# Kernel optimization log

Hardware: AMD Instinct MI355X
Metric: run time of the kernel (lower is better)

The kernel has to match this reference:

```python
import jax, jax.numpy as jnp
import numpy as np

POOL_RAD = 1.0   # init kwarg pool_rad
N = 16384        # total points
B = 8            # graphs in batch
F = 128          # feature dim
BIG = 1e30

def _voxel_keys(pos, batch, rad):
    # torch_geometric.voxel_grid with start=min-rad/2, end=max+rad/2, batch as extra dim
    start = pos.min(0) - rad * 0.5
    end = pos.max(0) + rad * 0.5
    nv = jnp.floor((end - start) / rad).astype(jnp.int32) + 1  # voxels per spatial dim
    c = jnp.floor((pos - start) / rad).astype(jnp.int32)       # [N,3] voxel coords
    lin = c[:, 0] + c[:, 1] * nv[0] + c[:, 2] * nv[0] * nv[1]
    return lin + batch.astype(jnp.int32) * (nv[0] * nv[1] * nv[2])

def _consecutive(keys, n):
    # consecutive_cluster: relabel to sorted-consecutive ids; perm = last index per cluster
    _, inv = jnp.unique(keys, return_inverse=True, size=n,
                        fill_value=jnp.iinfo(jnp.int32).max)
    inv = inv.reshape(-1)
    perm = jax.ops.segment_max(jnp.arange(n, dtype=jnp.int32), inv, num_segments=n)
    counts = jax.ops.segment_sum(jnp.ones((n,), jnp.int32), inv, num_segments=n)
    return inv, jnp.clip(perm, 0, n - 1), counts

def _nearest(pos, batch, cpos, cbatch, cvalid):
    # nearest centroid within the same graph; invalid/padded centroids masked out
    d = (pos * pos).sum(1)[:, None] - 2.0 * (pos @ cpos.T) + (cpos * cpos).sum(1)[None, :]
    ok = (batch[:, None] == cbatch[None, :]) & cvalid[None, :]
    return jnp.argmin(jnp.where(ok, d, BIG), axis=1)

def _pool(pos, x, batch):
    n = pos.shape[0]
    # stage 1: voxel-grid clustering, centroid positions
    inv1, perm1, cnt1 = _consecutive(_voxel_keys(pos, batch, POOL_RAD), n)
    c1 = jnp.maximum(cnt1, 1).astype(pos.dtype)[:, None]
    cpos = jax.ops.segment_sum(pos, inv1, num_segments=n) / c1
    cbatch = batch[perm1]
    # stage 2: reassign each point to its nearest voxel centroid, relabel
    cl2 = _nearest(jax.lax.stop_gradient(pos), batch,
                   jax.lax.stop_gradient(cpos), cbatch, cnt1 > 0)
    inv2, perm2, cnt2 = _consecutive(cl2, n)
    valid2 = cnt2 > 0
    c2 = jnp.maximum(cnt2, 1).astype(pos.dtype)[:, None]
    pos_out = jax.ops.segment_sum(pos, inv2, num_segments=n) / c2   # mean pos
    x_out = jax.ops.segment_max(x, inv2, num_segments=n)            # aggr='max'
    x_out = jnp.where(valid2[:, None], x_out, 0.0)
    pos_out = jnp.where(valid2[:, None], pos_out, 0.0)
    batch_out = jnp.where(valid2, batch[perm2], -1)
    return x_out, pos_out, batch_out

def setup_inputs():
    key = jax.random.key(0)
    k1, k2 = jax.random.split(key)
    pos = jax.random.uniform(k1, (N, 3), jnp.float32) * 10.0
    x = jax.random.normal(k2, (N, F), jnp.float32)
    batch = jnp.repeat(jnp.arange(B, dtype=jnp.int32), N // B)
    return {"pos": pos, "x": x, "batch": batch}

def reference(pos, x, batch):
    return _pool(pos, x, batch)
```

## Files before the change

### kernel.cpp

```cpp
#include <hip/hip_runtime.h>

#define TPB 256
#define K1SZ 32768

static __device__ __forceinline__ unsigned int fmap(float f) {
  unsigned int b = __float_as_uint(f);
  return (b & 0x80000000u) ? ~b : (b | 0x80000000u);
}
static __device__ __forceinline__ float funmap(unsigned int u) {
  unsigned int b = (u & 0x80000000u) ? (u & 0x7fffffffu) : ~u;
  return __uint_as_float(b);
}

static __device__ __forceinline__ int wave_incl_scan(int v, int lane) {
  #pragma unroll
  for (int off = 1; off < 64; off <<= 1) {
    int u = __shfl_up(v, off);
    if (lane >= off) v += u;
  }
  return v;
}

__global__ void k_init(double* __restrict__ sum1, double* __restrict__ sum2,
                       int* __restrict__ cnt1, int* __restrict__ cnt2,
                       int* __restrict__ perm2, int* __restrict__ flags1,
                       int* __restrict__ flags2, uint4* __restrict__ xacc4,
                       const float* __restrict__ pos, const int* __restrict__ batch,
                       float* __restrict__ scal, int n, int nF4) {
  int t = blockIdx.x * blockDim.x + threadIdx.x;
  if (t < nF4) xacc4[t] = uint4{0u, 0u, 0u, 0u};
  if (t < 3 * n) { sum1[t] = 0.0; sum2[t] = 0.0; }
  if (t < n) { cnt1[t] = 0; cnt2[t] = 0; perm2[t] = -1; flags2[t] = 0; }
  if (t < K1SZ) flags1[t] = 0;

  if (blockIdx.x == 0) {
    const int tid = threadIdx.x;
    const int lane = tid & 63, wid = tid >> 6;
    float mn[3] = {3.4e38f, 3.4e38f, 3.4e38f};
    float mx[3] = {-3.4e38f, -3.4e38f, -3.4e38f};
    int mb = 0;
    const float4* p4 = (const float4*)pos;
    const int4* b4 = (const int4*)batch;
    int np4 = n >> 2;
    for (int j = tid; j < np4; j += TPB) {
      float4 a = p4[3 * j], b = p4[3 * j + 1], c = p4[3 * j + 2];
      mn[0] = fminf(mn[0], fminf(fminf(a.x, a.w), fminf(b.z, c.y)));
      mx[0] = fmaxf(mx[0], fmaxf(fmaxf(a.x, a.w), fmaxf(b.z, c.y)));
      mn[1] = fminf(mn[1], fminf(fminf(a.y, b.x), fminf(b.w, c.z)));
      mx[1] = fmaxf(mx[1], fmaxf(fmaxf(a.y, b.x), fmaxf(b.w, c.z)));
      mn[2] = fminf(mn[2], fminf(fminf(a.z, b.y), fminf(c.x, c.w)));
      mx[2] = fmaxf(mx[2], fmaxf(fmaxf(a.z, b.y), fmaxf(c.x, c.w)));
      int4 bb = b4[j];
      mb = max(mb, max(max(bb.x, bb.y), max(bb.z, bb.w)));
    }
    if (tid == 0) {
      for (int i = np4 * 4; i < n; ++i) {
        for (int d = 0; d < 3; ++d) {
          float v = pos[i * 3 + d];
          mn[d] = fminf(mn[d], v);
          mx[d] = fmaxf(mx[d], v);
        }
        mb = max(mb, batch[i]);
      }
    }
    #pragma unroll
    for (int off = 32; off > 0; off >>= 1) {
      #pragma unroll
      for (int d = 0; d < 3; ++d) {
        mn[d] = fminf(mn[d], __shfl_xor(mn[d], off));
        mx[d] = fmaxf(mx[d], __shfl_xor(mx[d], off));
      }
      mb = max(mb, __shfl_xor(mb, off));
    }
    __shared__ float smn[4][3], smx[4][3];
    __shared__ int smb[4];
    if (lane == 0) {
      for (int d = 0; d < 3; ++d) { smn[wid][d] = mn[d]; smx[wid][d] = mx[d]; }
      smb[wid] = mb;
    }
    __syncthreads();
    if (tid == 0) {
      float rmn[3], rmx[3];
      int rmb = smb[0];
      for (int d = 0; d < 3; ++d) { rmn[d] = smn[0][d]; rmx[d] = smx[0][d]; }
      for (int w = 1; w < 4; ++w) {
        for (int d = 0; d < 3; ++d) {
          rmn[d] = fminf(rmn[d], smn[w][d]);
          rmx[d] = fmaxf(rmx[d], smx[w][d]);
        }
        rmb = max(rmb, smb[w]);
      }
      int nv[3];
      for (int d = 0; d < 3; ++d) {
        float start = rmn[d] - 0.5f;
        float end   = rmx[d] + 0.5f;
        nv[d] = (int)floorf(end - start) + 1;
        scal[d] = start;
      }
      int* isc = (int*)(scal + 3);
      isc[0] = nv[0];
      isc[1] = nv[0] * nv[1];
      isc[2] = nv[0] * nv[1] * nv[2];
      isc[3] = nv[1];
      isc[4] = nv[2];
      isc[5] = rmb + 1;
    }
  }
}

__global__ void k_keys(const float* __restrict__ pos, const int* __restrict__ batch, int n,
                       const float* __restrict__ scal, int* __restrict__ key1,
                       int* __restrict__ flags1) {
  int i = blockIdx.x * blockDim.x + threadIdx.x;
  if (i >= n) return;
  const int* isc = (const int*)(scal + 3);
  int c0 = (int)floorf(pos[i * 3 + 0] - scal[0]);
  int c1 = (int)floorf(pos[i * 3 + 1] - scal[1]);
  int c2 = (int)floorf(pos[i * 3 + 2] - scal[2]);
  int key = c0 + c1 * isc[0] + c2 * isc[1] + batch[i] * isc[2];
  key = min(max(key, 0), K1SZ - 1);
  key1[i] = key;
  flags1[key] = 1;
}

static __device__ __forceinline__ int scan_body(const int* __restrict__ flags,
                                                int* __restrict__ rank,
                                                int ntiles, int n4full, int* wsum) {
  const int t = threadIdx.x;
  const int lane = t & 63;
  const int wid = t >> 6;
  const int4* f4 = (const int4*)flags;
  int4* r4 = (int4*)rank;
  int base = 0;
  for (int tile = 0; tile < ntiles; ++tile) {
    int i = tile * 1024 + t;
    int4 v = (i < n4full) ? f4[i] : int4{0, 0, 0, 0};
    int q0 = v.x, q1 = q0 + v.y, q2 = q1 + v.z, q3 = q2 + v.w;
    int ws = wave_incl_scan(q3, lane);
    if (lane == 63) wsum[wid] = ws;
    __syncthreads();
    int woff = 0, ttot = 0;
    #pragma unroll
    for (int w = 0; w < 16; ++w) {
      int s = wsum[w];
      if (w < wid) woff += s;
      ttot += s;
    }
    int e = base + woff + (ws - q3);
    if (i < n4full) r4[i] = int4{e, e + q0, e + q1, e + q2};
    base += ttot;
    __syncthreads();
  }
  return base;
}

__global__ __launch_bounds__(1024) void k_scan1(const int* __restrict__ flags,
                                                int* __restrict__ rank,
                                                const float* __restrict__ scal) {
  __shared__ int wsum[16];
  const int* isc = (const int*)(scal + 3);
  long long L = (long long)isc[5] * isc[2];
  int L_eff = (int)(L > K1SZ ? K1SZ : L);
  int ntiles = (L_eff + 4095) >> 12;
  int base = scan_body(flags, rank, ntiles, K1SZ >> 2, wsum);
  if (threadIdx.x == 0) rank[K1SZ] = base;
}

__global__ __launch_bounds__(1024) void k_scan2(const int* __restrict__ flags,
                                                int* __restrict__ rank,
                                                const int* __restrict__ total1, int n) {
  __shared__ int wsum[16];
  int L_eff = min(n, *total1);
  int ntiles = (L_eff + 4095) >> 12;
  scan_body(flags, rank, ntiles, n >> 2, wsum);
}

__global__ void k_assign1(const float* __restrict__ pos, int n,
                          const int* __restrict__ key1, const int* __restrict__ rank1,
                          int* __restrict__ cnt1, double* __restrict__ sum1) {
  int i = blockIdx.x * blockDim.x + threadIdx.x;
  if (i >= n) return;
  int c = rank1[key1[i]];
  atomicAdd(&cnt1[c], 1);
  atomicAdd(&sum1[c * 3 + 0], (double)pos[i * 3 + 0]);
  atomicAdd(&sum1[c * 3 + 1], (double)pos[i * 3 + 1]);
  atomicAdd(&sum1[c * 3 + 2], (double)pos[i * 3 + 2]);
}

__global__ void k_nearest(const float* __restrict__ pos, const int* __restrict__ batch, int n,
                          const double* __restrict__ sum1, const int* __restrict__ cnt1,
                          const int* __restrict__ flags1, const int* __restrict__ rank1,
                          const float* __restrict__ scal,
                          int* __restrict__ cl2, int* __restrict__ flags2) {
  int i = blockIdx.x * blockDim.x + threadIdx.x;
  if (i >= n) return;
  const int* isc = (const int*)(scal + 3);
  const float s0 = scal[0], s1 = scal[1], s2 = scal[2];
  const int nv0 = isc[0], nv01 = isc[1], nvtot = isc[2];
  const int nv1 = isc[3], nv2 = isc[4];
  float pxf = pos[i * 3 + 0], pyf = pos[i * 3 + 1], pzf = pos[i * 3 + 2];
  double px = pxf, py = pyf, pz = pzf;
  int c0 = (int)floorf(pxf - s0);
  int c1 = (int)floorf(pyf - s1);
  int c2 = (int)floorf(pzf - s2);
  int base = batch[i] * nvtot;
  int k0 = min(max(c0 + c1 * nv0 + c2 * nv01 + base, 0), K1SZ - 1);
  int bid = rank1[k0];
  {
    double inv = 1.0 / (double)cnt1[bid];
    double dx = px - sum1[bid * 3 + 0] * inv;
    double dy = py - sum1[bid * 3 + 1] * inv;
    double dz = pz - sum1[bid * 3 + 2] * inv;
    double d2 = dx * dx + dy * dy + dz * dz;
    double best2 = d2;
    for (int oz = -2; oz <= 2; ++oz) {
      int z = c2 + oz;
      if (z < 0 || z >= nv2) continue;
      double lz = (double)s2 + z;
      double gz = fmax(0.0, fmax(lz - pz, pz - (lz + 1.0)));
      double gz2 = gz * gz;
      if (gz2 > best2 + 1e-4) continue;
      for (int oy = -2; oy <= 2; ++oy) {
        int y = c1 + oy;
        if (y < 0 || y >= nv1) continue;
        double ly = (double)s1 + y;
        double gy = fmax(0.0, fmax(ly - py, py - (ly + 1.0)));
        double gzy2 = gz2 + gy * gy;
        if (gzy2 > best2 + 1e-4) continue;
        for (int ox = -2; ox <= 2; ++ox) {
          int xq = c0 + ox;
          if (xq < 0 || xq >= nv0) continue;
          if ((ox | oy | oz) == 0) continue;
          double lx = (double)s0 + xq;
          double gx = fmax(0.0, fmax(lx - px, px - (lx + 1.0)));
          double mind2 = gzy2 + gx * gx;
          if (mind2 > best2 + 1e-4) continue;
          int key = min(xq + y * nv0 + z * nv01 + base, K1SZ - 1);
          if (!flags1[key]) continue;
          int c = rank1[key];
          double cinv = 1.0 / (double)cnt1[c];
          double ddx = px - sum1[c * 3 + 0] * cinv;
          double ddy = py - sum1[c * 3 + 1] * cinv;
          double ddz = pz - sum1[c * 3 + 2] * cinv;
          double dd2 = ddx * ddx + ddy * ddy + ddz * ddz;
          if (dd2 < best2 || (dd2 == best2 && c < bid)) { best2 = dd2; bid = c; }
        }
      }
    }
  }
  cl2[i] = bid;
  flags2[bid] = 1;
}

__global__ void k_assign2_xmax(const float* __restrict__ pos, const float4* __restrict__ x4,
                               int n, int F4, int F, const int* __restrict__ cl2,
                               const int* __restrict__ rank2, int* __restrict__ cnt2,
                               int* __restrict__ perm2, double* __restrict__ sum2,
                               unsigned int* __restrict__ xacc) {
  int t = blockIdx.x * blockDim.x + threadIdx.x;
  if (t >= n * F4) return;
  int i = t / F4;
  int q = t - i * F4;
  int c = rank2[cl2[i]];
  float4 v = x4[t];
  unsigned int* dst = &xacc[c * F + q * 4];
  atomicMax(dst + 0, fmap(v.x));
  atomicMax(dst + 1, fmap(v.y));
  atomicMax(dst + 2, fmap(v.z));
  atomicMax(dst + 3, fmap(v.w));
  if (q == 0) {
    atomicAdd(&cnt2[c], 1);
    atomicMax(&perm2[c], i);
    atomicAdd(&sum2[c * 3 + 0], (double)pos[i * 3 + 0]);
    atomicAdd(&sum2[c * 3 + 1], (double)pos[i * 3 + 1]);
    atomicAdd(&sum2[c * 3 + 2], (double)pos[i * 3 + 2]);
  }
}

__global__ void k_finalize(int n, int F4, const int* __restrict__ cnt2,
                           const int* __restrict__ perm2, const int* __restrict__ batch,
                           const double* __restrict__ sum2, uint4* __restrict__ xacc4,
                           float* __restrict__ pos_out, float* __restrict__ batch_out) {
  int t = blockIdx.x * blockDim.x + threadIdx.x;
  if (t < n * F4) {
    int j = t / F4;
    float4 o = {0.0f, 0.0f, 0.0f, 0.0f};
    if (cnt2[j] > 0) {
      uint4 v = xacc4[t];
      o.x = funmap(v.x); o.y = funmap(v.y); o.z = funmap(v.z); o.w = funmap(v.w);
    }
    ((float4*)xacc4)[t] = o;
  }
  if (t < n) {
    int c = cnt2[t];
    if (c > 0) {
      double inv = 1.0 / (double)c;
      pos_out[t * 3 + 0] = (float)(sum2[t * 3 + 0] * inv);
      pos_out[t * 3 + 1] = (float)(sum2[t * 3 + 1] * inv);
      pos_out[t * 3 + 2] = (float)(sum2[t * 3 + 2] * inv);
      batch_out[t] = (float)batch[perm2[t]];
    } else {
      pos_out[t * 3 + 0] = 0.0f;
      pos_out[t * 3 + 1] = 0.0f;
      pos_out[t * 3 + 2] = 0.0f;
      batch_out[t] = -1.0f;
    }
  }
}

extern "C" void kernel_launch(void* const* d_in, const int* in_sizes, int n_in,
                              void* d_out, int out_size, void* d_ws, size_t ws_size,
                              hipStream_t stream) {
  const float* pos   = (const float*)d_in[0];
  const float* x     = (const float*)d_in[1];
  const int*   batch = (const int*)d_in[2];
  int n = in_sizes[2];
  int F = in_sizes[1] / n;
  int F4 = F >> 2;
  int nF4 = n * F4;

  char* ws = (char*)d_ws;
  size_t off = 0;
  auto alloc = [&](size_t bytes, size_t align) -> void* {
    off = (off + align - 1) & ~(align - 1);
    void* p = ws + off;
    off += bytes;
    return p;
  };
  double* sum1   = (double*)alloc((size_t)n * 3 * sizeof(double), 16);
  double* sum2   = (double*)alloc((size_t)n * 3 * sizeof(double), 16);
  int* key1      = (int*)alloc((size_t)n * 4, 16);
  int* cl2       = (int*)alloc((size_t)n * 4, 16);
  int* cnt1      = (int*)alloc((size_t)n * 4, 16);
  int* cnt2      = (int*)alloc((size_t)n * 4, 16);
  int* perm2     = (int*)alloc((size_t)n * 4, 16);
  int* flags1    = (int*)alloc((size_t)K1SZ * 4, 16);
  int* rank1     = (int*)alloc(((size_t)K1SZ + 4) * 4, 16);
  int* flags2    = (int*)alloc((size_t)n * 4, 16);
  int* rank2     = (int*)alloc((size_t)n * 4, 16);
  float* scal    = (float*)alloc(64, 16);

  unsigned int* xacc = (unsigned int*)d_out;
  float* pos_out     = (float*)d_out + (size_t)n * F;
  float* batch_out   = pos_out + (size_t)n * 3;

  int nb   = (n + TPB - 1) / TPB;
  int nbV  = (nF4 + TPB - 1) / TPB;
  int nbP  = (n + 63) / 64;

  k_init<<<nbV, TPB, 0, stream>>>(sum1, sum2, cnt1, cnt2, perm2, flags1, flags2,
                                  (uint4*)xacc, pos, batch, scal, n, nF4);
  k_keys<<<nb, TPB, 0, stream>>>(pos, batch, n, scal, key1, flags1);
  k_scan1<<<1, 1024, 0, stream>>>(flags1, rank1, scal);
  k_assign1<<<nb, TPB, 0, stream>>>(pos, n, key1, rank1, cnt1, sum1);
  k_nearest<<<nbP, 64, 0, stream>>>(pos, batch, n, sum1, cnt1, flags1, rank1, scal,
                                    cl2, flags2);
  k_scan2<<<1, 1024, 0, stream>>>(flags2, rank2, rank1 + K1SZ, n);
  k_assign2_xmax<<<nbV, TPB, 0, stream>>>(pos, (const float4*)x, n, F4, F, cl2, rank2,
                                          cnt2, perm2, sum2, xacc);
  k_finalize<<<nbV, TPB, 0, stream>>>(n, F4, cnt2, perm2, batch, sum2,
                                      (uint4*)xacc, pos_out, batch_out);
}
```

Measured before the change: 72.60 us.

## Drop stage-1 compaction scan and accumulate centroids directly by voxel key

Stage-1 centroid sums and counts are now accumulated straight into arrays indexed by the raw voxel key. This removes the key buffer, the flags1/rank1 arrays, the first single-block scan, and the separate assign kernel. The nearest-centroid search tests occupancy with cnt1 and breaks ties by voxel key, which gives the same order as the old compacted rank. The second scan now runs over the key space (up to 32768 entries) with a 256-thread block instead of over n with 1024 threads. That shortens the launch chain but may make the serial scan longer, and sum1/cnt1/flags2 grow to K1SZ entries that k_init must zero.

```diff
diff --git a/kernel.cpp b/kernel.cpp
--- a/kernel.cpp
+++ b/kernel.cpp
@@ -23,15 +23,16 @@
 
 __global__ void k_init(double* __restrict__ sum1, double* __restrict__ sum2,
                        int* __restrict__ cnt1, int* __restrict__ cnt2,
-                       int* __restrict__ perm2, int* __restrict__ flags1,
-                       int* __restrict__ flags2, uint4* __restrict__ xacc4,
+                       int* __restrict__ perm2, int* __restrict__ flags2,
+                       uint4* __restrict__ xacc4,
                        const float* __restrict__ pos, const int* __restrict__ batch,
                        float* __restrict__ scal, int n, int nF4) {
   int t = blockIdx.x * blockDim.x + threadIdx.x;
   if (t < nF4) xacc4[t] = uint4{0u, 0u, 0u, 0u};
-  if (t < 3 * n) { sum1[t] = 0.0; sum2[t] = 0.0; }
-  if (t < n) { cnt1[t] = 0; cnt2[t] = 0; perm2[t] = -1; flags2[t] = 0; }
-  if (t < K1SZ) flags1[t] = 0;
+  if (t < 3 * K1SZ) sum1[t] = 0.0;
+  if (t < 3 * n) sum2[t] = 0.0;
+  if (t < K1SZ) { cnt1[t] = 0; flags2[t] = 0; }
+  if (t < n) { cnt2[t] = 0; perm2[t] = -1; }
 
   if (blockIdx.x == 0) {
     const int tid = threadIdx.x;
@@ -43,15 +44,15 @@
     const int4* b4 = (const int4*)batch;
     int np4 = n >> 2;
     for (int j = tid; j < np4; j += TPB) {
-      float4 a = p4[3 * j], b = p4[3 * j + 1], c = p4[3 * j + 2];
-      mn[0] = fminf(mn[0], fminf(fminf(a.x, a.w), fminf(b.z, c.y)));
-      mx[0] = fmaxf(mx[0], fmaxf(fmaxf(a.x, a.w), fmaxf(b.z, c.y)));
-      mn[1] = fminf(mn[1], fminf(fminf(a.y, b.x), fminf(b.w, c.z)));
-      mx[1] = fmaxf(mx[1], fmaxf(fmaxf(a.y, b.x), fmaxf(b.w, c.z)));
-      mn[2] = fminf(mn[2], fminf(fminf(a.z, b.y), fminf(c.x, c.w)));
-      mx[2] = fmaxf(mx[2], fmaxf(fmaxf(a.z, b.y), fmaxf(c.x, c.w)));
-      int4 bb = b4[j];
-      mb = max(mb, max(max(bb.x, bb.y), max(bb.z, bb.w)));
+      float4 aa = p4[3 * j], bb = p4[3 * j + 1], cc = p4[3 * j + 2];
+      mn[0] = fminf(mn[0], fminf(fminf(aa.x, aa.w), fminf(bb.z, cc.y)));
+      mx[0] = fmaxf(mx[0], fmaxf(fmaxf(aa.x, aa.w), fmaxf(bb.z, cc.y)));
+      mn[1] = fminf(mn[1], fminf(fminf(aa.y, bb.x), fminf(bb.w, cc.z)));
+      mx[1] = fmaxf(mx[1], fmaxf(fmaxf(aa.y, bb.x), fmaxf(bb.w, cc.z)));
+      mn[2] = fminf(mn[2], fminf(fminf(aa.z, bb.y), fminf(cc.x, cc.w)));
+      mx[2] = fmaxf(mx[2], fmaxf(fmaxf(aa.z, bb.y), fmaxf(cc.x, cc.w)));
+      int4 q = b4[j];
+      mb = max(mb, max(max(q.x, q.y), max(q.z, q.w)));
     }
     if (tid == 0) {
       for (int i = np4 * 4; i < n; ++i) {
@@ -108,88 +109,26 @@
   }
 }
 
-__global__ void k_keys(const float* __restrict__ pos, const int* __restrict__ batch, int n,
-                       const float* __restrict__ scal, int* __restrict__ key1,
-                       int* __restrict__ flags1) {
+__global__ void k_keyacc(const float* __restrict__ pos, const int* __restrict__ batch,
+                         int n, const float* __restrict__ scal,
+                         int* __restrict__ cnt1, double* __restrict__ sum1) {
   int i = blockIdx.x * blockDim.x + threadIdx.x;
   if (i >= n) return;
   const int* isc = (const int*)(scal + 3);
-  int c0 = (int)floorf(pos[i * 3 + 0] - scal[0]);
-  int c1 = (int)floorf(pos[i * 3 + 1] - scal[1]);
-  int c2 = (int)floorf(pos[i * 3 + 2] - scal[2]);
+  float px = pos[i * 3 + 0], py = pos[i * 3 + 1], pz = pos[i * 3 + 2];
+  int c0 = (int)floorf(px - scal[0]);
+  int c1 = (int)floorf(py - scal[1]);
+  int c2 = (int)floorf(pz - scal[2]);
   int key = c0 + c1 * isc[0] + c2 * isc[1] + batch[i] * isc[2];
   key = min(max(key, 0), K1SZ - 1);
-  key1[i] = key;
-  flags1[key] = 1;
-}
-
-static __device__ __forceinline__ int scan_body(const int* __restrict__ flags,
-                                                int* __restrict__ rank,
-                                                int ntiles, int n4full, int* wsum) {
-  const int t = threadIdx.x;
-  const int lane = t & 63;
-  const int wid = t >> 6;
-  const int4* f4 = (const int4*)flags;
-  int4* r4 = (int4*)rank;
-  int base = 0;
-  for (int tile = 0; tile < ntiles; ++tile) {
-    int i = tile * 1024 + t;
-    int4 v = (i < n4full) ? f4[i] : int4{0, 0, 0, 0};
-    int q0 = v.x, q1 = q0 + v.y, q2 = q1 + v.z, q3 = q2 + v.w;
-    int ws = wave_incl_scan(q3, lane);
-    if (lane == 63) wsum[wid] = ws;
-    __syncthreads();
-    int woff = 0, ttot = 0;
-    #pragma unroll
-    for (int w = 0; w < 16; ++w) {
-      int s = wsum[w];
-      if (w < wid) woff += s;
-      ttot += s;
-    }
-    int e = base + woff + (ws - q3);
-    if (i < n4full) r4[i] = int4{e, e + q0, e + q1, e + q2};
-    base += ttot;
-    __syncthreads();
-  }
-  return base;
-}
-
-__global__ __launch_bounds__(1024) void k_scan1(const int* __restrict__ flags,
-                                                int* __restrict__ rank,
-                                                const float* __restrict__ scal) {
-  __shared__ int wsum[16];
-  const int* isc = (const int*)(scal + 3);
-  long long L = (long long)isc[5] * isc[2];
-  int L_eff = (int)(L > K1SZ ? K1SZ : L);
-  int ntiles = (L_eff + 4095) >> 12;
-  int base = scan_body(flags, rank, ntiles, K1SZ >> 2, wsum);
-  if (threadIdx.x == 0) rank[K1SZ] = base;
-}
-
-__global__ __launch_bounds__(1024) void k_scan2(const int* __restrict__ flags,
-                                                int* __restrict__ rank,
-                                                const int* __restrict__ total1, int n) {
-  __shared__ int wsum[16];
-  int L_eff = min(n, *total1);
-  int ntiles = (L_eff + 4095) >> 12;
-  scan_body(flags, rank, ntiles, n >> 2, wsum);
-}
-
-__global__ void k_assign1(const float* __restrict__ pos, int n,
-                          const int* __restrict__ key1, const int* __restrict__ rank1,
-                          int* __restrict__ cnt1, double* __restrict__ sum1) {
-  int i = blockIdx.x * blockDim.x + threadIdx.x;
-  if (i >= n) return;
-  int c = rank1[key1[i]];
-  atomicAdd(&cnt1[c], 1);
-  atomicAdd(&sum1[c * 3 + 0], (double)pos[i * 3 + 0]);
-  atomicAdd(&sum1[c * 3 + 1], (double)pos[i * 3 + 1]);
-  atomicAdd(&sum1[c * 3 + 2], (double)pos[i * 3 + 2]);
+  atomicAdd(&cnt1[key], 1);
+  atomicAdd(&sum1[key * 3 + 0], (double)px);
+  atomicAdd(&sum1[key * 3 + 1], (double)py);
+  atomicAdd(&sum1[key * 3 + 2], (double)pz);
 }
 
 __global__ void k_nearest(const float* __restrict__ pos, const int* __restrict__ batch, int n,
                           const double* __restrict__ sum1, const int* __restrict__ cnt1,
-                          const int* __restrict__ flags1, const int* __restrict__ rank1,
                           const float* __restrict__ scal,
                           int* __restrict__ cl2, int* __restrict__ flags2) {
   int i = blockIdx.x * blockDim.x + threadIdx.x;
@@ -204,52 +143,83 @@
   int c1 = (int)floorf(pyf - s1);
   int c2 = (int)floorf(pzf - s2);
   int base = batch[i] * nvtot;
-  int k0 = min(max(c0 + c1 * nv0 + c2 * nv01 + base, 0), K1SZ - 1);
-  int bid = rank1[k0];
-  {
-    double inv = 1.0 / (double)cnt1[bid];
-    double dx = px - sum1[bid * 3 + 0] * inv;
-    double dy = py - sum1[bid * 3 + 1] * inv;
-    double dz = pz - sum1[bid * 3 + 2] * inv;
-    double d2 = dx * dx + dy * dy + dz * dz;
-    double best2 = d2;
-    for (int oz = -2; oz <= 2; ++oz) {
-      int z = c2 + oz;
-      if (z < 0 || z >= nv2) continue;
-      double lz = (double)s2 + z;
-      double gz = fmax(0.0, fmax(lz - pz, pz - (lz + 1.0)));
-      double gz2 = gz * gz;
-      if (gz2 > best2 + 1e-4) continue;
-      for (int oy = -2; oy <= 2; ++oy) {
-        int y = c1 + oy;
-        if (y < 0 || y >= nv1) continue;
-        double ly = (double)s1 + y;
-        double gy = fmax(0.0, fmax(ly - py, py - (ly + 1.0)));
-        double gzy2 = gz2 + gy * gy;
-        if (gzy2 > best2 + 1e-4) continue;
-        for (int ox = -2; ox <= 2; ++ox) {
-          int xq = c0 + ox;
-          if (xq < 0 || xq >= nv0) continue;
-          if ((ox | oy | oz) == 0) continue;
-          double lx = (double)s0 + xq;
-          double gx = fmax(0.0, fmax(lx - px, px - (lx + 1.0)));
-          double mind2 = gzy2 + gx * gx;
-          if (mind2 > best2 + 1e-4) continue;
-          int key = min(xq + y * nv0 + z * nv01 + base, K1SZ - 1);
-          if (!flags1[key]) continue;
-          int c = rank1[key];
-          double cinv = 1.0 / (double)cnt1[c];
-          double ddx = px - sum1[c * 3 + 0] * cinv;
-          double ddy = py - sum1[c * 3 + 1] * cinv;
-          double ddz = pz - sum1[c * 3 + 2] * cinv;
-          double dd2 = ddx * ddx + ddy * ddy + ddz * ddz;
-          if (dd2 < best2 || (dd2 == best2 && c < bid)) { best2 = dd2; bid = c; }
-        }
-      }
-    }
-  }
-  cl2[i] = bid;
-  flags2[bid] = 1;
+  int bkey = min(max(c0 + c1 * nv0 + c2 * nv01 + base, 0), K1SZ - 1);
+  double inv = 1.0 / (double)cnt1[bkey];
+  double dx = px - sum1[bkey * 3 + 0] * inv;
+  double dy = py - sum1[bkey * 3 + 1] * inv;
+  double dz = pz - sum1[bkey * 3 + 2] * inv;
+  double best2 = dx * dx + dy * dy + dz * dz;
+  for (int oz = -2; oz <= 2; ++oz) {
+    int z = c2 + oz;
+    if (z < 0 || z >= nv2) continue;
+    double lz = (double)s2 + z;
+    double gz = fmax(0.0, fmax(lz - pz, pz - (lz + 1.0)));
+    double gz2 = gz * gz;
+    if (gz2 > best2 + 1e-4) continue;
+    for (int oy = -2; oy <= 2; ++oy) {
+      int y = c1 + oy;
+      if (y < 0 || y >= nv1) continue;
+      double ly = (double)s1 + y;
+      double gy = fmax(0.0, fmax(ly - py, py - (ly + 1.0)));
+      double gzy2 = gz2 + gy * gy;
+      if (gzy2 > best2 + 1e-4) continue;
+      for (int ox = -2; ox <= 2; ++ox) {
+        int xq = c0 + ox;
+        if (xq < 0 || xq >= nv0) continue;
+        if ((ox | oy | oz) == 0) continue;
+        double lx = (double)s0 + xq;
+        double gx = fmax(0.0, fmax(lx - px, px - (lx + 1.0)));
+        double mind2 = gzy2 + gx * gx;
+        if (mind2 > best2 + 1e-4) continue;
+        int key = min(xq + y * nv0 + z * nv01 + base, K1SZ - 1);
+        int c = cnt1[key];
+        if (c == 0) continue;
+        double cinv = 1.0 / (double)c;
+        double ddx = px - sum1[key * 3 + 0] * cinv;
+        double ddy = py - sum1[key * 3 + 1] * cinv;
+        double ddz = pz - sum1[key * 3 + 2] * cinv;
+        double dd2 = ddx * ddx + ddy * ddy + ddz * ddz;
+        if (dd2 < best2 || (dd2 == best2 && key < bkey)) { best2 = dd2; bkey = key; }
+      }
+    }
+  }
+  cl2[i] = bkey;
+  flags2[bkey] = 1;
+}
+
+__global__ __launch_bounds__(TPB) void k_scan2(const int* __restrict__ flags,
+                                               int* __restrict__ rank,
+                                               const float* __restrict__ scal) {
+  __shared__ int wsum[4];
+  const int t = threadIdx.x;
+  const int lane = t & 63, wid = t >> 6;
+  const int* isc = (const int*)(scal + 3);
+  long long L = (long long)isc[5] * isc[2];
+  int L_eff = (int)(L > K1SZ ? K1SZ : L);
+  int ntiles = (L_eff + TPB * 4 - 1) / (TPB * 4);
+  const int4* f4 = (const int4*)flags;
+  int4* r4 = (int4*)rank;
+  const int n4full = K1SZ >> 2;
+  int base = 0;
+  for (int tile = 0; tile < ntiles; ++tile) {
+    int i = tile * TPB + t;
+    int4 v = (i < n4full) ? f4[i] : int4{0, 0, 0, 0};
+    int q0 = v.x, q1 = q0 + v.y, q2 = q1 + v.z, q3 = q2 + v.w;
+    int ws = wave_incl_scan(q3, lane);
+    if (lane == 63) wsum[wid] = ws;
+    __syncthreads();
+    int woff = 0, ttot = 0;
+    #pragma unroll
+    for (int w = 0; w < 4; ++w) {
+      int s = wsum[w];
+      if (w < wid) woff += s;
+      ttot += s;
+    }
+    int e = base + woff + (ws - q3);
+    if (i < n4full) r4[i] = int4{e, e + q0, e + q1, e + q2};
+    base += ttot;
+    __syncthreads();
+  }
 }
 
 __global__ void k_assign2_xmax(const float* __restrict__ pos, const float4* __restrict__ x4,
@@ -263,7 +233,7 @@
   int q = t - i * F4;
   int c = rank2[cl2[i]];
   float4 v = x4[t];
-  unsigned int* dst = &xacc[c * F + q * 4];
+  unsigned int* dst = &xacc[(size_t)c * F + q * 4];
   atomicMax(dst + 0, fmap(v.x));
   atomicMax(dst + 1, fmap(v.y));
   atomicMax(dst + 2, fmap(v.z));
@@ -327,35 +297,29 @@
     off += bytes;
     return p;
   };
-  double* sum1   = (double*)alloc((size_t)n * 3 * sizeof(double), 16);
+  double* sum1   = (double*)alloc((size_t)K1SZ * 3 * sizeof(double), 16);
   double* sum2   = (double*)alloc((size_t)n * 3 * sizeof(double), 16);
-  int* key1      = (int*)alloc((size_t)n * 4, 16);
   int* cl2       = (int*)alloc((size_t)n * 4, 16);
-  int* cnt1      = (int*)alloc((size_t)n * 4, 16);
+  int* cnt1      = (int*)alloc((size_t)K1SZ * 4, 16);
   int* cnt2      = (int*)alloc((size_t)n * 4, 16);
   int* perm2     = (int*)alloc((size_t)n * 4, 16);
-  int* flags1    = (int*)alloc((size_t)K1SZ * 4, 16);
-  int* rank1     = (int*)alloc(((size_t)K1SZ + 4) * 4, 16);
-  int* flags2    = (int*)alloc((size_t)n * 4, 16);
-  int* rank2     = (int*)alloc((size_t)n * 4, 16);
+  int* flags2    = (int*)alloc((size_t)K1SZ * 4, 16);
+  int* rank2     = (int*)alloc((size_t)K1SZ * 4, 16);
   float* scal    = (float*)alloc(64, 16);
 
   unsigned int* xacc = (unsigned int*)d_out;
   float* pos_out     = (float*)d_out + (size_t)n * F;
   float* batch_out   = pos_out + (size_t)n * 3;
 
-  int nb   = (n + TPB - 1) / TPB;
-  int nbV  = (nF4 + TPB - 1) / TPB;
-  int nbP  = (n + 63) / 64;
-
-  k_init<<<nbV, TPB, 0, stream>>>(sum1, sum2, cnt1, cnt2, perm2, flags1, flags2,
+  int nb  = (n + TPB - 1) / TPB;
+  int nbV = (nF4 + TPB - 1) / TPB;
+  int nbP = (n + 63) / 64;
+
+  k_init<<<nbV, TPB, 0, stream>>>(sum1, sum2, cnt1, cnt2, perm2, flags2,
                                   (uint4*)xacc, pos, batch, scal, n, nF4);
-  k_keys<<<nb, TPB, 0, stream>>>(pos, batch, n, scal, key1, flags1);
-  k_scan1<<<1, 1024, 0, stream>>>(flags1, rank1, scal);
-  k_assign1<<<nb, TPB, 0, stream>>>(pos, n, key1, rank1, cnt1, sum1);
-  k_nearest<<<nbP, 64, 0, stream>>>(pos, batch, n, sum1, cnt1, flags1, rank1, scal,
-                                    cl2, flags2);
-  k_scan2<<<1, 1024, 0, stream>>>(flags2, rank2, rank1 + K1SZ, n);
+  k_keyacc<<<nb, TPB, 0, stream>>>(pos, batch, n, scal, cnt1, sum1);
+  k_nearest<<<nbP, 64, 0, stream>>>(pos, batch, n, sum1, cnt1, scal, cl2, flags2);
+  k_scan2<<<1, TPB, 0, stream>>>(flags2, rank2, scal);
   k_assign2_xmax<<<nbV, TPB, 0, stream>>>(pos, (const float4*)x, n, F4, F, cl2, rank2,
                                           cnt2, perm2, sum2, xacc);
   k_finalize<<<nbV, TPB, 0, stream>>>(n, F4, cnt2, perm2, batch, sum2,
```

New measurement: 68.82 us. 1.05x faster.
